# Optimization experiments

Hardware: AMD Instinct MI355X
Metric: run time of the kernel (lower is better)

## Reference

```python
import jax, jax.numpy as jnp
import numpy as np

NUM_FIELDS = 40
EMBED_DIM = 16

# Precompute static gather indices equivalent to the two masked_select calls.
# triu mask on a (F, F-1) grid, diagonal=0 -> pairs (i, j) with j >= i.
_tri = np.triu(np.ones((NUM_FIELDS, NUM_FIELDS - 1), dtype=np.int64), 0).astype(bool)
_I0, _J0 = np.nonzero(_tri)  # row-major order matches torch.masked_select
# tril(ones(F, F-1), -1).T -> (F-1, F) mask applied to x.transpose(1, 2).
_trl = np.tril(np.ones((NUM_FIELDS, NUM_FIELDS - 1), dtype=np.int64), -1).T.astype(bool)
_I1, _J1 = np.nonzero(_trl)  # indices into the transposed view
I0 = jnp.asarray(_I0); J0 = jnp.asarray(_J0)
I1 = jnp.asarray(_I1); J1 = jnp.asarray(_J1)


def setup_inputs() -> dict:
    key = jax.random.key(0)
    bs = 2048
    inputs = jax.random.normal(key, (bs, NUM_FIELDS * (NUM_FIELDS - 1) * EMBED_DIM), dtype=jnp.float32)
    return {"inputs": inputs}


def reference(inputs):
    bs = inputs.shape[0]
    F = NUM_FIELDS
    # [bs, F, F-1, D]
    x = inputs.reshape(bs, F, F - 1, -1)
    # emb0 = masked_select(x, triu_mask): gather pairs in row-major order
    emb0 = x[:, I0, J0, :]            # [bs, P, D], P = F*(F-1)/2
    # emb1 = masked_select(x.transpose(1,2), tril_mask): xt[b,a,c,:] = x[b,c,a,:]
    emb1 = x[:, J1, I1, :]            # [bs, P, D]
    # (emb0*emb1).view(bs,-1).sum(-1)
    return jnp.einsum('bpd,bpd->b', emb0, emb1)
```

## Files before the change

### kernel.cpp

```cpp
#include <hip/hip_runtime.h>


#define NF 40
#define NC 39
#define ED 16
#define NPAIRS 780
#define ROW_FLOATS (NF * NC * ED)
#define NTASKS (NPAIRS * 4)
#define NTH 512
#define TRIPS ((NTASKS + NTH - 1) / NTH)

typedef float f32x4 __attribute__((ext_vector_type(4)));

__global__ __launch_bounds__(NTH) void ffm_interact_kernel(
        const float* __restrict__ x, float* __restrict__ out) {
    const int n = blockIdx.x;
    const int tid = threadIdx.x;
    const int q = tid & 3;
    const int p0 = tid >> 2;
    const f32x4* __restrict__ base4 =
        (const f32x4*)(x + (size_t)n * ROW_FLOATS);

    int aoff[TRIPS], boff[TRIPS];
    #pragma unroll
    for (int k = 0; k < TRIPS; ++k) {
        int p = p0 + 128 * k;
        p = p < NPAIRS ? p : (NPAIRS - 1);
        const float disc = 6241.0f - 8.0f * (float)p;
        int i = (int)((79.0f - __builtin_sqrtf(disc)) * 0.5f);
        int Si = 39 * i - ((i * (i - 1)) >> 1);
        if (p < Si) { --i; Si = 39 * i - ((i * (i - 1)) >> 1); }
        else { const int Si1 = Si + (NC - i); if (p >= Si1) { ++i; Si = Si1; } }
        const int j = i + (p - Si);
        aoff[k] = (i * NC + j) * 4 + q;
        boff[k] = ((j + 1) * NC + i) * 4 + q;
    }

    f32x4 av[TRIPS], bv[TRIPS];
    #pragma unroll
    for (int k = 0; k < TRIPS; ++k)
        av[k] = __builtin_nontemporal_load(&base4[aoff[k]]);
    #pragma unroll
    for (int k = 0; k < TRIPS; ++k)
        bv[k] = __builtin_nontemporal_load(&base4[boff[k]]);

    float acc = 0.0f;
    #pragma unroll
    for (int k = 0; k < TRIPS; ++k) {
        const float m = ((tid + k * NTH) < NTASKS) ? 1.0f : 0.0f;
        acc = fmaf(m * av[k][0], bv[k][0], acc);
        acc = fmaf(m * av[k][1], bv[k][1], acc);
        acc = fmaf(m * av[k][2], bv[k][2], acc);
        acc = fmaf(m * av[k][3], bv[k][3], acc);
    }

    #pragma unroll
    for (int off = 32; off > 0; off >>= 1)
        acc += __shfl_down(acc, off, 64);

    __shared__ float wave_sum[NTH / 64];
    if ((tid & 63) == 0) wave_sum[tid >> 6] = acc;
    __syncthreads();
    if (tid == 0) {
        float s = 0.0f;
        #pragma unroll
        for (int w = 0; w < NTH / 64; ++w) s += wave_sum[w];
        out[n] = s;
    }
}

extern "C" void kernel_launch(void* const* d_in, const int* in_sizes, int n_in,
                              void* d_out, int out_size, void* d_ws, size_t ws_size,
                              hipStream_t stream) {
    const float* x = (const float*)d_in[0];
    float* out = (float*)d_out;
    const int bs = in_sizes[0] / ROW_FLOATS;
    ffm_interact_kernel<<<bs, NTH, 0, stream>>>(x, out);
}
```

Baseline: 257.5 us.

## Stream each row coalesced and pair partners through shared memory

```diff
diff --git a/kernel.cpp b/kernel.cpp
--- a/kernel.cpp
+++ b/kernel.cpp
@@ -6,9 +6,9 @@
 #define ED 16
 #define NPAIRS 780
 #define ROW_FLOATS (NF * NC * ED)
-#define NTASKS (NPAIRS * 4)
+#define ROW_F4 (ROW_FLOATS / 4)
 #define NTH 512
-#define TRIPS ((NTASKS + NTH - 1) / NTH)
+#define TRIPS ((ROW_F4 + NTH - 1) / NTH)
 
 typedef float f32x4 __attribute__((ext_vector_type(4)));
 
@@ -16,42 +16,49 @@
         const float* __restrict__ x, float* __restrict__ out) {
     const int n = blockIdx.x;
     const int tid = threadIdx.x;
-    const int q = tid & 3;
-    const int p0 = tid >> 2;
     const f32x4* __restrict__ base4 =
         (const f32x4*)(x + (size_t)n * ROW_FLOATS);
 
-    int aoff[TRIPS], boff[TRIPS];
+    __shared__ f32x4 bslot[NPAIRS * 4];
+
+    f32x4 v[TRIPS];
     #pragma unroll
     for (int k = 0; k < TRIPS; ++k) {
-        int p = p0 + 128 * k;
-        p = p < NPAIRS ? p : (NPAIRS - 1);
-        const float disc = 6241.0f - 8.0f * (float)p;
-        int i = (int)((79.0f - __builtin_sqrtf(disc)) * 0.5f);
-        int Si = 39 * i - ((i * (i - 1)) >> 1);
-        if (p < Si) { --i; Si = 39 * i - ((i * (i - 1)) >> 1); }
-        else { const int Si1 = Si + (NC - i); if (p >= Si1) { ++i; Si = Si1; } }
-        const int j = i + (p - Si);
-        aoff[k] = (i * NC + j) * 4 + q;
-        boff[k] = ((j + 1) * NC + i) * 4 + q;
+        const int g = tid + k * NTH;
+        if (g < ROW_F4) v[k] = base4[g];
     }
 
-    f32x4 av[TRIPS], bv[TRIPS];
+    int aidx[TRIPS];
     #pragma unroll
-    for (int k = 0; k < TRIPS; ++k)
-        av[k] = __builtin_nontemporal_load(&base4[aoff[k]]);
-    #pragma unroll
-    for (int k = 0; k < TRIPS; ++k)
-        bv[k] = __builtin_nontemporal_load(&base4[boff[k]]);
+    for (int k = 0; k < TRIPS; ++k) {
+        const int g = tid + k * NTH;
+        aidx[k] = -1;
+        if (g < ROW_F4) {
+            const int c = g >> 2;
+            const int q = g & 3;
+            const int f = (int)((unsigned)c / NC);
+            const int cc = c - f * NC;
+            if (f <= cc) {
+                const int p = ((f * (79 - f)) >> 1) + (cc - f);
+                aidx[k] = p * 4 + q;
+            } else {
+                const int p = ((cc * (79 - cc)) >> 1) + (f - 1 - cc);
+                bslot[p * 4 + q] = v[k];
+            }
+        }
+    }
+    __syncthreads();
 
     float acc = 0.0f;
     #pragma unroll
     for (int k = 0; k < TRIPS; ++k) {
-        const float m = ((tid + k * NTH) < NTASKS) ? 1.0f : 0.0f;
-        acc = fmaf(m * av[k][0], bv[k][0], acc);
-        acc = fmaf(m * av[k][1], bv[k][1], acc);
-        acc = fmaf(m * av[k][2], bv[k][2], acc);
-        acc = fmaf(m * av[k][3], bv[k][3], acc);
+        if (aidx[k] >= 0) {
+            const f32x4 b = bslot[aidx[k]];
+            acc = fmaf(v[k][0], b[0], acc);
+            acc = fmaf(v[k][1], b[1], acc);
+            acc = fmaf(v[k][2], b[2], acc);
+            acc = fmaf(v[k][3], b[3], acc);
+        }
     }
 
     #pragma unroll
```

Measured after the change: 272.7 us. 1.06x slower.
